# Kernel tuning notes

Measured on AMD Instinct MI355X. Metric: run time of the kernel, lower is better.

## Reference

```python
import jax, jax.numpy as jnp
import numpy as np

N = 50000   # drug nodes
R = 8       # relations (= n_classes)
E = 200000  # edges per relation
ED = 400000 # decoder edges


def _deg_norm(idx, n):
    deg = jax.ops.segment_sum(jnp.ones(idx.shape, jnp.float32), idx, num_segments=n)
    return jnp.where(deg > 0, jax.lax.rsqrt(jnp.maximum(deg, 1.0)), 0.0)


def hetero_conv(x, src, dst, W, b, n):
    # DGL HeteroGraphConv(sum) of GraphConv(norm='both') per relation, single node type.
    out = jnp.zeros((n, W.shape[2]), x.dtype)
    for r in range(W.shape[0]):
        s, d = src[r], dst[r]
        ns = _deg_norm(s, n)  # out-degree^{-1/2} (src norm)
        nd = _deg_norm(d, n)  # in-degree^{-1/2} (dst norm)
        m = (x * ns[:, None]) @ W[r]                       # [n, dout]
        agg = jax.ops.segment_sum(m[s], d, num_segments=n)  # gather+scatter [E, dout]
        out = out + agg * nd[:, None] + b[r]
    return out


def hgcn_layer(x, src, dst, Wa, ba, Wb, bb, n):
    h = hetero_conv(x, src, dst, Wa, ba, n)
    h = jax.nn.relu(h)
    return hetero_conv(h, src, dst, Wb, bb, n)


def setup_inputs() -> dict:
    key = jax.random.key(0)
    ks = jax.random.split(key, 16)
    s = 0.02
    return {
        "node2_features": jax.random.normal(ks[0], (N, 256), jnp.float32),
        "mpnn_features": jax.random.normal(ks[1], (N, 300), jnp.float32),
        "src": jax.random.randint(ks[2], (R, E), 0, N, jnp.int32),
        "dst": jax.random.randint(ks[3], (R, E), 0, N, jnp.int32),
        "dec_src": jax.random.randint(ks[4], (ED,), 0, N, jnp.int32),
        "dec_dst": jax.random.randint(ks[5], (ED,), 0, N, jnp.int32),
        "W2a": jax.random.normal(ks[6], (R, 256, 256), jnp.float32) * s,
        "b2a": jnp.zeros((R, 256), jnp.float32),
        "W2b": jax.random.normal(ks[7], (R, 256, 128), jnp.float32) * s,
        "b2b": jnp.zeros((R, 128), jnp.float32),
        "W3a": jax.random.normal(ks[8], (R, 300, 256), jnp.float32) * s,
        "b3a": jnp.zeros((R, 256), jnp.float32),
        "W3b": jax.random.normal(ks[9], (R, 256, 128), jnp.float32) * s,
        "b3b": jnp.zeros((R, 128), jnp.float32),
        "Wp1": jax.random.normal(ks[10], (512, 256), jnp.float32) * s,
        "bp1": jnp.zeros((256,), jnp.float32),
        "Wp2": jax.random.normal(ks[11], (256, R), jnp.float32) * s,
        "bp2": jnp.zeros((R,), jnp.float32),
    }


def reference(node2_features, mpnn_features, src, dst, dec_src, dec_dst,
              W2a, b2a, W2b, b2b, W3a, b3a, W3b, b3b, Wp1, bp1, Wp2, bp2):
    h2 = hgcn_layer(node2_features, src, dst, W2a, b2a, W2b, b2b, N)  # [N, 128]
    h3 = hgcn_layer(mpnn_features, src, dst, W3a, b3a, W3b, b3b, N)   # [N, 128]
    feat = jnp.concatenate([h2, h3], axis=1)                            # [N, 256]
    # edge-wise gather-concat-MLP (note: original has NO relu between W1 and W2)
    x = jnp.concatenate([feat[dec_src], feat[dec_dst]], axis=1)          # [ED, 512]
    score = (x @ Wp1 + bp1) @ Wp2 + bp2                                  # [ED, R]
    return score
```

## Files before the change

### kernel.cpp

```cpp
#include <hip/hip_runtime.h>
#include <hip/hip_bf16.h>

#define NN 50000
#define RR 8
#define EE 200000
#define EDD 400000
#define SCB 196
#define CH 5000
#define CHK 16

typedef __attribute__((ext_vector_type(8))) short short8;
typedef __attribute__((ext_vector_type(4))) float floatx4;

static __device__ __forceinline__ unsigned short f2bf(float f) {
    union { float f; unsigned u; } v; v.f = f;
    unsigned r = v.u + 0x7fff + ((v.u >> 16) & 1);
    return (unsigned short)(r >> 16);
}
static __device__ __forceinline__ float bf2f(unsigned short h) {
    union { unsigned u; float f; } v; v.u = ((unsigned)h) << 16;
    return v.f;
}
static __device__ __forceinline__ void gload_lds16(const unsigned short* g, unsigned short* l) {
    __builtin_amdgcn_global_load_lds(
        (const __attribute__((address_space(1))) void*)g,
        (__attribute__((address_space(3))) void*)l,
        16, 0, 0);
}

__global__ __launch_bounds__(256) void k_histp(const int* __restrict__ src, const int* __restrict__ dst,
                                               unsigned char* __restrict__ tmp) {
    __shared__ unsigned lh[12512];
    int chunk = blockIdx.x, r = blockIdx.y, which = blockIdx.z;
    const int* idx = (which ? dst : src) + (size_t)r * EE;
    for (int i = threadIdx.x; i < 12512; i += 256) lh[i] = 0;
    __syncthreads();
    int e0 = chunk * (EE / CHK);
    for (int e = e0 + threadIdx.x; e < e0 + EE / CHK; e += 256) {
        int n = idx[e];
        atomicAdd(&lh[n >> 2], 1u << ((n & 3) * 8));
    }
    __syncthreads();
    unsigned* t = (unsigned*)(tmp + (((size_t)(which * RR + r) * CHK + chunk) * 50048));
    for (int i = threadIdx.x; i < 12512; i += 256) t[i] = lh[i];
}

__global__ void k_reduce(const unsigned char* __restrict__ tmp,
                         int* __restrict__ outdeg, int* __restrict__ indeg) {
    int i = blockIdx.x * 256 + threadIdx.x;
    if (i >= 2 * RR * 12512) return;
    int wr = i / 12512;
    int wd = i - wr * 12512;
    unsigned s0 = 0, s1 = 0, s2 = 0, s3 = 0;
    const unsigned* base = (const unsigned*)(tmp + (size_t)wr * CHK * 50048) + wd;
    #pragma unroll
    for (int c = 0; c < CHK; c++) {
        unsigned v = base[(size_t)c * 12512];
        s0 += v & 255u; s1 += (v >> 8) & 255u; s2 += (v >> 16) & 255u; s3 += (v >> 24) & 255u;
    }
    int which = wr / RR, r = wr - which * RR;
    int n = wd * 4;
    int* deg = (which ? indeg : outdeg) + (size_t)r * NN;
    if (n < NN) {
        deg[n] = (int)s0;
        if (n + 1 < NN) deg[n + 1] = (int)s1;
        if (n + 2 < NN) deg[n + 2] = (int)s2;
        if (n + 3 < NN) deg[n + 3] = (int)s3;
    }
}

__global__ void k_norms(int* __restrict__ outdeg, int* __restrict__ indeg) {
    int i = blockIdx.x * blockDim.x + threadIdx.x;
    if (i >= RR * NN) return;
    int od = outdeg[i];
    int id = indeg[i];
    ((float*)outdeg)[i] = od > 0 ? rsqrtf((float)od) : 0.f;
    ((float*)indeg)[i]  = id > 0 ? rsqrtf((float)id) : 0.f;
}

__global__ void k_scanA(const int* __restrict__ indeg, int* __restrict__ bsum) {
    int r = blockIdx.y;
    int i = blockIdx.x * 256 + threadIdx.x;
    int v = (i < NN) ? indeg[(size_t)r * NN + i] : 0;
    #pragma unroll
    for (int d = 32; d > 0; d >>= 1) v += __shfl_down(v, d, 64);
    __shared__ int ws4[4];
    if ((threadIdx.x & 63) == 0) ws4[threadIdx.x >> 6] = v;
    __syncthreads();
    if (threadIdx.x == 0) bsum[r * SCB + blockIdx.x] = ws4[0] + ws4[1] + ws4[2] + ws4[3];
}

__global__ void k_scanB(int* __restrict__ bsum, int* __restrict__ offs) {
    int r = blockIdx.x;
    int t = threadIdx.x;
    int v = (t < SCB) ? bsum[r * SCB + t] : 0;
    int lane = t & 63, wid = t >> 6;
    int sv = v;
    #pragma unroll
    for (int d = 1; d < 64; d <<= 1) {
        int u = __shfl_up(sv, d, 64);
        if (lane >= d) sv += u;
    }
    __shared__ int wsum[4];
    if (lane == 63) wsum[wid] = sv;
    __syncthreads();
    int add = 0;
    for (int x = 0; x < wid; x++) add += wsum[x];
    int incl = sv + add;
    if (t < SCB) bsum[r * SCB + t] = incl - v;
    if (t == 255) offs[(size_t)r * (NN + 1) + NN] = incl;
}

__global__ void k_scanC(const int* __restrict__ indeg, const int* __restrict__ bsum,
                        int* __restrict__ offs) {
    int r = blockIdx.y;
    int i = blockIdx.x * 256 + threadIdx.x;
    int v = (i < NN) ? indeg[(size_t)r * NN + i] : 0;
    int lane = threadIdx.x & 63, wid = threadIdx.x >> 6;
    int sv = v;
    #pragma unroll
    for (int d = 1; d < 64; d <<= 1) {
        int u = __shfl_up(sv, d, 64);
        if (lane >= d) sv += u;
    }
    __shared__ int wsum[4];
    if (lane == 63) wsum[wid] = sv;
    __syncthreads();
    int add = bsum[r * SCB + blockIdx.x];
    for (int x = 0; x < wid; x++) add += wsum[x];
    if (i < NN) offs[(size_t)r * (NN + 1) + i] = sv - v + add;
}

__global__ void k_fillw(const int* __restrict__ src, const int* __restrict__ dst,
                        const int* __restrict__ offs, const float* __restrict__ ns,
                        int* __restrict__ cursor, int2* __restrict__ csrw) {
    int i = blockIdx.x * blockDim.x + threadIdx.x;
    if (i >= RR * EE) return;
    int r = i / EE;
    int s = src[i], d = dst[i];
    int pos = offs[r * (NN + 1) + d] + atomicAdd(&cursor[r * NN + d], 1);
    int2 v;
    v.x = s;
    v.y = __float_as_int(ns[(size_t)r * NN + s]);
    csrw[(size_t)r * EE + pos] = v;
}

__global__ void k_prep(const float* __restrict__ Wp1, const float* __restrict__ Wp2,
                       const float* __restrict__ bp1, const float* __restrict__ bp2,
                       const float* __restrict__ b2a, const float* __restrict__ b2b,
                       const float* __restrict__ b3a, const float* __restrict__ b3b,
                       float* __restrict__ Mcat, float* __restrict__ cvec,
                       float* __restrict__ bs) {
    int bx = blockIdx.x;
    if (bx < 16) {
        int t = bx * 256 + threadIdx.x;
        int i = t >> 4, j = t & 15;
        int half = j >> 3, jj = j & 7;
        const float* wrow = Wp1 + (size_t)(half * 256 + i) * 256;
        float s = 0.f;
        for (int k = 0; k < 256; k++) s += wrow[k] * Wp2[k * 8 + jj];
        Mcat[i * 16 + j] = s;
    } else if (bx == 16) {
        int j = threadIdx.x;
        if (j < 8) {
            float s = bp2[j];
            for (int k = 0; k < 256; k++) s += bp1[k] * Wp2[k * 8 + j];
            cvec[j] = s;
        }
    } else {
        int j = threadIdx.x;
        float s = 0.f;
        for (int r = 0; r < RR; r++) s += b2a[r * 256 + j];
        bs[j] = s;
        if (j < 128) {
            s = 0.f;
            for (int r = 0; r < RR; r++) s += b2b[r * 128 + j];
            bs[256 + j] = s;
        }
        s = 0.f;
        for (int r = 0; r < RR; r++) s += b3a[r * 256 + j];
        bs[512 + j] = s;
        if (j < 128) {
            s = 0.f;
            for (int r = 0; r < RR; r++) s += b3b[r * 128 + j];
            bs[768 + j] = s;
        }
    }
}

__global__ void k_fold(const float* __restrict__ W2b, const float* __restrict__ W3b,
                       const float* __restrict__ Mcat, const float* __restrict__ bs,
                       unsigned short* __restrict__ FmatT, float* __restrict__ cfold) {
    int bx = blockIdx.x;
    if (bx < 256) {
        int idx = bx * 256 + threadIdx.x;
        int rj = idx >> 9, i = idx & 511;
        int r = rj >> 4, j = rj & 15;
        float s = 0.f;
        if (i < 256) {
            const float* wr = W2b + ((size_t)r * 256 + i) * 128;
            for (int c = 0; c < 128; c++) s += wr[c] * Mcat[c * 16 + j];
        } else {
            const float* wr = W3b + ((size_t)r * 256 + (i - 256)) * 128;
            for (int c = 0; c < 128; c++) s += wr[c] * Mcat[(128 + c) * 16 + j];
        }
        FmatT[(size_t)rj * 512 + i] = f2bf(s);
    } else {
        int j = threadIdx.x;
        if (j < 16) {
            float s = 0.f;
            for (int c = 0; c < 128; c++)
                s += bs[256 + c] * Mcat[c * 16 + j] + bs[768 + c] * Mcat[(128 + c) * 16 + j];
            cfold[j] = s;
        }
    }
}

__global__ void k_castx(const float* __restrict__ x2, const float* __restrict__ x3,
                        unsigned short* __restrict__ XH) {
    int i = blockIdx.x * 256 + threadIdx.x;
    if (i >= NN * 560) return;
    int row = i / 560, col = i - row * 560;
    float v;
    if (col < 256) v = x2[(size_t)row * 256 + col];
    else if (col < 556) v = x3[(size_t)row * 300 + (col - 256)];
    else v = 0.f;
    XH[i] = f2bf(v);
}

__global__ void k_wt2(const float* __restrict__ W2a, const float* __restrict__ W3a,
                      unsigned short* __restrict__ WT2, unsigned short* __restrict__ WT3) {
    const float* W; unsigned short* WT; int K0, Kpad;
    if (blockIdx.y == 0) { W = W2a; WT = WT2; K0 = 256; Kpad = 256; }
    else                 { W = W3a; WT = WT3; K0 = 300; Kpad = 304; }
    int i = blockIdx.x * 256 + threadIdx.x;
    int total = 256 * RR * Kpad;
    if (i >= total) return;
    int n = i / (RR * Kpad);
    int rem = i - n * (RR * Kpad);
    int r = rem / Kpad;
    int k = rem - r * Kpad;
    float v = (k < K0) ? W[((size_t)r * K0 + k) * 256 + n] : 0.f;
    WT[i] = f2bf(v);
}

__global__ __launch_bounds__(256) void k_aggp(
        const unsigned short* __restrict__ xb,
        const int2* __restrict__ csrw, const int* __restrict__ offs,
        const float* __restrict__ nd, int nbase,
        unsigned short* __restrict__ Y2, unsigned short* __restrict__ Y3) {
    int lane = threadIdx.x & 63;
    int sub = threadIdx.x >> 6;
    int bn = blockIdx.x * 4 + sub;
    int n = nbase + bn;
    int r = blockIdx.y;
    int o0 = offs[r * (NN + 1) + n];
    int o1 = offs[r * (NN + 1) + n + 1];
    o0 = __builtin_amdgcn_readfirstlane(o0);
    o1 = __builtin_amdgcn_readfirstlane(o1);
    int cnt = o1 - o0;
    float ndv = nd[(size_t)r * NN + n];
    const int2* cs = csrw + (size_t)r * EE + o0;
    bool tl = lane < 6;
    float va[8], vc[8];
    #pragma unroll
    for (int q = 0; q < 8; q++) { va[q] = 0.f; vc[q] = 0.f; }

    for (int eb = 0; eb < cnt; eb += 64) {
        int rem = cnt - eb;
        int2 rec = cs[eb + min(lane, rem - 1)];
        int kmax = rem < 64 ? rem : 64;
        for (int kb = 0; kb < kmax; kb += 4) {
            #pragma unroll
            for (int u = 0; u < 4; u++) {
                int k = kb + u;
                if (k >= kmax) break;
                int sidx = __shfl(rec.x, k, 64);
                float f = __int_as_float(__shfl(rec.y, k, 64));
                const unsigned short* p = xb + (size_t)(unsigned)sidx * 560;
                short8 M = *(const short8*)(p + lane * 8);
                #pragma unroll
                for (int q = 0; q < 8; q++) va[q] += f * bf2f((unsigned short)M[q]);
                if (tl) {
                    short8 C = *(const short8*)(p + 512 + lane * 8);
                    #pragma unroll
                    for (int q = 0; q < 8; q++) vc[q] += f * bf2f((unsigned short)C[q]);
                }
            }
        }
    }
    short8 o;
    #pragma unroll
    for (int q = 0; q < 8; q++) o[q] = (short)f2bf(va[q] * ndv);
    if (lane < 32) {
        *(short8*)(Y2 + (size_t)bn * 2048 + r * 256 + lane * 8) = o;
    } else {
        *(short8*)(Y3 + (size_t)bn * 2432 + r * 304 + (lane - 32) * 8) = o;
    }
    if (tl) {
        short8 oc;
        #pragma unroll
        for (int q = 0; q < 8; q++) oc[q] = (short)f2bf(vc[q] * ndv);
        *(short8*)(Y3 + (size_t)bn * 2432 + r * 304 + 256 + lane * 8) = oc;
    }
}

template<int TN>
__global__ __launch_bounds__(256) void k_gemm_bf(
        const unsigned short* __restrict__ A, int lda,
        const unsigned short* __restrict__ BT, int ldb,
        const float* __restrict__ bias,
        const float* __restrict__ Cin, int ldcin,
        void* __restrict__ Cout, int ldc,
        int M, int K, int flags) {
    constexpr int BN = TN * 32;
    __shared__ unsigned short As[128 * 64];
    __shared__ unsigned short Bs[BN * 64];
    int m0 = blockIdx.x * 128;
    int n0 = blockIdx.y * BN;
    int t = threadIdx.x;
    int w = t >> 6, l = t & 63;
    int qm = (w >> 1) * 64, qn = (w & 1) * (TN * 16);
    int lr = l & 15, lg = l >> 4;
    int lrow = l >> 3;
    int lch  = (l & 7) ^ lrow;

    floatx4 acc[4][TN];
    #pragma unroll
    for (int a = 0; a < 4; a++)
        #pragma unroll
        for (int b = 0; b < TN; b++)
            acc[a][b] = (floatx4){0.f, 0.f, 0.f, 0.f};

    for (int k0 = 0; k0 < K; k0 += 64) {
        #pragma unroll
        for (int j = 0; j < 4; j++) {
            int seg = w * 4 + j;
            int gr = m0 + seg * 8 + lrow; if (gr > M - 1) gr = M - 1;
            gload_lds16(A + (size_t)gr * lda + k0 + lch * 8, &As[seg * 512]);
        }
        #pragma unroll
        for (int j = 0; j < TN; j++) {
            int seg = w * TN + j;
            int row = n0 + seg * 8 + lrow;
            gload_lds16(BT + (size_t)row * ldb + k0 + lch * 8, &Bs[seg * 512]);
        }
        __syncthreads();
        #pragma unroll
        for (int ks = 0; ks < 2; ks++) {
            int slot = ((ks * 4 + lg) ^ (lr & 7)) * 8;
            short8 af[4], bf[TN];
            #pragma unroll
            for (int i = 0; i < 4; i++)
                af[i] = *(const short8*)&As[(qm + i * 16 + lr) * 64 + slot];
            #pragma unroll
            for (int i = 0; i < TN; i++)
                bf[i] = *(const short8*)&Bs[(qn + i * 16 + lr) * 64 + slot];
            #pragma unroll
            for (int tm = 0; tm < 4; tm++)
                #pragma unroll
                for (int tn = 0; tn < TN; tn++)
                    acc[tm][tn] = __builtin_amdgcn_mfma_f32_16x16x32_bf16(
                        af[tm], bf[tn], acc[tm][tn], 0, 0, 0);
        }
        __syncthreads();
    }

    int addbias = flags & 1, accum = flags & 2, relu = flags & 4, outbf = flags & 8;
    #pragma unroll
    for (int tm = 0; tm < 4; tm++) {
        int rbase = m0 + qm + tm * 16 + lg * 4;
        #pragma unroll
        for (int reg = 0; reg < 4; reg++) {
            int row = rbase + reg;
            if (row >= M) continue;
            #pragma unroll
            for (int tn = 0; tn < TN; tn++) {
                int col = n0 + qn + tn * 16 + lr;
                float v = acc[tm][tn][reg];
                if (addbias) v += bias[col];
                if (accum) v += Cin[(size_t)row * ldcin + col];
                if (relu) v = fmaxf(v, 0.f);
                if (outbf) ((unsigned short*)Cout)[(size_t)row * ldc + col] = f2bf(v);
                else       ((float*)Cout)[(size_t)row * ldc + col] = v;
            }
        }
    }
}

__global__ __launch_bounds__(256) void k_gemm2(
        const unsigned short* __restrict__ Y2, const unsigned short* __restrict__ Y3,
        const unsigned short* __restrict__ WT2, const unsigned short* __restrict__ WT3,
        const float* __restrict__ bs, unsigned short* __restrict__ hb,
        int nbase, int M) {
    __shared__ unsigned short As[64 * 64];
    __shared__ unsigned short Bs[64 * 64];
    int x = blockIdx.x;
    int g = (x >> 5) * 8 + (x & 7);
    int nb = (x >> 3) & 3;
    if (g >= 158) return;
    int z = g / 79;
    int mb = g - z * 79;
    const unsigned short* A  = z ? Y3 : Y2;
    const unsigned short* BT = z ? WT3 : WT2;
    int lda = z ? 2432 : 2048;
    int K = lda;
    const float* bias = bs + z * 512;
    int m0 = mb * 64;
    int n0 = nb * 64;
    int t = threadIdx.x;
    int w = t >> 6, l = t & 63;
    int qm = (w >> 1) * 32, qn = (w & 1) * 32;
    int lr = l & 15, lg = l >> 4;
    int lrow = l >> 3;
    int lch  = (l & 7) ^ lrow;

    floatx4 acc[2][2];
    #pragma unroll
    for (int a = 0; a < 2; a++)
        #pragma unroll
        for (int b = 0; b < 2; b++)
            acc[a][b] = (floatx4){0.f, 0.f, 0.f, 0.f};

    for (int k0 = 0; k0 < K; k0 += 64) {
        #pragma unroll
        for (int j = 0; j < 2; j++) {
            int seg = w * 2 + j;
            int gr = m0 + seg * 8 + lrow; if (gr > M - 1) gr = M - 1;
            gload_lds16(A + (size_t)gr * lda + k0 + lch * 8, &As[seg * 512]);
        }
        #pragma unroll
        for (int j = 0; j < 2; j++) {
            int seg = w * 2 + j;
            int row = n0 + seg * 8 + lrow;
            gload_lds16(BT + (size_t)row * lda + k0 + lch * 8, &Bs[seg * 512]);
        }
        __syncthreads();
        #pragma unroll
        for (int ks = 0; ks < 2; ks++) {
            int slot = ((ks * 4 + lg) ^ (lr & 7)) * 8;
            short8 af[2], bf[2];
            #pragma unroll
            for (int i = 0; i < 2; i++)
                af[i] = *(const short8*)&As[(qm + i * 16 + lr) * 64 + slot];
            #pragma unroll
            for (int i = 0; i < 2; i++)
                bf[i] = *(const short8*)&Bs[(qn + i * 16 + lr) * 64 + slot];
            #pragma unroll
            for (int tm = 0; tm < 2; tm++)
                #pragma unroll
                for (int tn = 0; tn < 2; tn++)
                    acc[tm][tn] = __builtin_amdgcn_mfma_f32_16x16x32_bf16(
                        af[tm], bf[tn], acc[tm][tn], 0, 0, 0);
        }
        __syncthreads();
    }

    #pragma unroll
    for (int tm = 0; tm < 2; tm++) {
        int rbase = m0 + qm + tm * 16 + lg * 4;
        #pragma unroll
        for (int reg = 0; reg < 4; reg++) {
            int row = rbase + reg;
            if (row >= M) continue;
            #pragma unroll
            for (int tn = 0; tn < 2; tn++) {
                int col = n0 + qn + tn * 16 + lr;
                float v = fmaxf(acc[tm][tn][reg] + bias[col], 0.f);
                hb[(size_t)(nbase + row) * 512 + z * 256 + col] = f2bf(v);
            }
        }
    }
}

__global__ __launch_bounds__(256) void k_aggAB(
        const int2* __restrict__ csrw, const int* __restrict__ offs,
        const float* __restrict__ nd, const float* __restrict__ G,
        const float* __restrict__ cfold, const float* __restrict__ cvec,
        float* __restrict__ AB) {
    int lane = threadIdx.x & 63, sub = threadIdx.x >> 6;
    int n = blockIdx.x * 4 + sub;
    int slot = lane >> 4, j = lane & 15;
    int jb = slot << 4;
    float acc = 0.f;
    for (int hh = 0; hh < 2; hh++) {
        int r = slot + hh * 4;
        int o0 = offs[r * (NN + 1) + n];
        int o1 = offs[r * (NN + 1) + n + 1];
        float ndv = nd[(size_t)r * NN + n];
        const int2* cs = csrw + (size_t)r * EE + o0;
        int cnt = o1 - o0;
        float t0 = 0.f, t1 = 0.f;
        for (int eb = 0; eb < cnt; eb += 16) {
            int rem = cnt - eb;
            int2 rec = cs[eb + min(j, rem - 1)];
            int kmax = rem < 16 ? rem : 16;
            for (int k = 0; k < kmax; k += 2) {
                int s0 = __shfl(rec.x, jb + k, 64);
                float f0 = __int_as_float(__shfl(rec.y, jb + k, 64));
                int k1 = k + 1 < kmax ? k + 1 : kmax - 1;
                int s1 = __shfl(rec.x, jb + k1, 64);
                float f1 = (k + 1 < kmax) ? __int_as_float(__shfl(rec.y, jb + k1, 64)) : 0.f;
                t0 += f0 * G[(size_t)(unsigned)s0 * 128 + r * 16 + j];
                t1 += f1 * G[(size_t)(unsigned)s1 * 128 + r * 16 + j];
            }
        }
        acc += ndv * (t0 + t1);
    }
    acc += __shfl_xor(acc, 16, 64);
    acc += __shfl_xor(acc, 32, 64);
    if (lane < 16) AB[(size_t)n * 16 + j] = acc + cfold[j] + (j < 8 ? cvec[j] : 0.f);
}

__global__ void k_dec(const int* __restrict__ dsrc, const int* __restrict__ ddst,
                      const float* __restrict__ AB, float* __restrict__ out) {
    int e = blockIdx.x * 256 + threadIdx.x;
    if (e >= EDD) return;
    int s = dsrc[e], d = ddst[e];
    const float4* as = (const float4*)(AB + (size_t)s * 16);
    const float4* ad = (const float4*)(AB + (size_t)d * 16 + 8);
    float4 x0 = as[0], x1 = as[1], y0 = ad[0], y1 = ad[1];
    float4 o0 = {x0.x + y0.x, x0.y + y0.y, x0.z + y0.z, x0.w + y0.w};
    float4 o1 = {x1.x + y1.x, x1.y + y1.y, x1.z + y1.z, x1.w + y1.w};
    float4* op = (float4*)(out + (size_t)e * 8);
    op[0] = o0; op[1] = o1;
}

extern "C" void kernel_launch(void* const* d_in, const int* in_sizes, int n_in,
                              void* d_out, int out_size, void* d_ws, size_t ws_size,
                              hipStream_t stream) {
    const float* x2  = (const float*)d_in[0];
    const float* x3  = (const float*)d_in[1];
    const int*   src = (const int*)d_in[2];
    const int*   dst = (const int*)d_in[3];
    const int*   dsrc = (const int*)d_in[4];
    const int*   ddst = (const int*)d_in[5];
    const float* W2a = (const float*)d_in[6];
    const float* b2a = (const float*)d_in[7];
    const float* W2b = (const float*)d_in[8];
    const float* b2b = (const float*)d_in[9];
    const float* W3a = (const float*)d_in[10];
    const float* b3a = (const float*)d_in[11];
    const float* W3b = (const float*)d_in[12];
    const float* b3b = (const float*)d_in[13];
    const float* Wp1 = (const float*)d_in[14];
    const float* bp1 = (const float*)d_in[15];
    const float* Wp2 = (const float*)d_in[16];
    const float* bp2 = (const float*)d_in[17];
    float* out = (float*)d_out;

    char* ws = (char*)d_ws;
    size_t off = 0;
    auto alloc = [&](size_t nbytes) {
        char* p = ws + off;
        off += nbytes;
        off = (off + 255) & ~(size_t)255;
        return p;
    };
    float* ns   = (float*)alloc((size_t)RR * NN * 4);
    float* nd   = (float*)alloc((size_t)RR * NN * 4);
    int*   offs = (int*)alloc((size_t)RR * (NN + 1) * 4);
    int2*  csrw = (int2*)alloc((size_t)RR * EE * 8);
    unsigned short* XH     = (unsigned short*)alloc((size_t)NN * 560 * 2);
    unsigned short* hbuf23 = (unsigned short*)alloc((size_t)NN * 512 * 2);
    unsigned short* WT2a   = (unsigned short*)alloc((size_t)256 * 2048 * 2);
    unsigned short* WT3a   = (unsigned short*)alloc((size_t)256 * 2432 * 2);
    unsigned short* FmatT  = (unsigned short*)alloc((size_t)128 * 512 * 2);
    char* YR = alloc((size_t)CH * (2048 + 2432) * 2);
    float* Mcat  = (float*)alloc(4096 * 4);
    float* cvec  = (float*)alloc(64 * 4);
    float* bsums = (float*)alloc(1024 * 4);
    float* cfold = (float*)alloc(64 * 4);
    int*   bsum  = (int*)alloc((size_t)RR * SCB * 4);

    unsigned short* Y2a = (unsigned short*)YR;
    unsigned short* Y3a = Y2a + (size_t)CH * 2048;
    int*   outdeg = (int*)ns;
    int*   indeg  = (int*)nd;
    int*   cursor = (int*)YR;
    unsigned char* htmp = (unsigned char*)(YR + (4 << 20));
    float* G      = (float*)YR;
    float* AB     = (float*)(YR + (size_t)NN * 128 * 4);

    hipMemsetAsync(cursor, 0, (size_t)RR * NN * 4, stream);

    k_histp<<<dim3(CHK, RR, 2), 256, 0, stream>>>(src, dst, htmp);
    k_reduce<<<(2 * RR * 12512 + 255) / 256, 256, 0, stream>>>(htmp, outdeg, indeg);
    k_scanA<<<dim3(SCB, RR), 256, 0, stream>>>(indeg, bsum);
    k_scanB<<<RR, 256, 0, stream>>>(bsum, offs);
    k_scanC<<<dim3(SCB, RR), 256, 0, stream>>>(indeg, bsum, offs);
    k_norms<<<(RR * NN + 255) / 256, 256, 0, stream>>>(outdeg, indeg);
    int edgeBlocks = (RR * EE + 255) / 256;
    k_fillw<<<edgeBlocks, 256, 0, stream>>>(src, dst, offs, ns, cursor, csrw);
    k_prep<<<18, 256, 0, stream>>>(Wp1, Wp2, bp1, bp2, b2a, b2b, b3a, b3b, Mcat, cvec, bsums);
    k_fold<<<257, 256, 0, stream>>>(W2b, W3b, Mcat, bsums, FmatT, cfold);

    k_castx<<<(NN * 560 + 255) / 256, 256, 0, stream>>>(x2, x3, XH);
    k_wt2<<<dim3((256 * RR * 304 + 255) / 256, 2), 256, 0, stream>>>(W2a, W3a, WT2a, WT3a);

    for (int c = 0; c < NN / CH; c++) {
        k_aggp<<<dim3(CH / 4, RR), 256, 0, stream>>>(XH, csrw, offs, nd, c * CH, Y2a, Y3a);
        k_gemm2<<<640, 256, 0, stream>>>(
            Y2a, Y3a, WT2a, WT3a, bsums, hbuf23, c * CH, CH);
    }

    k_gemm_bf<1><<<dim3((NN + 127) / 128, 4), 256, 0, stream>>>(
        hbuf23, 512, FmatT, 512, bsums, (const float*)nullptr, 0,
        (void*)G, 128, NN, 512, 0);

    k_aggAB<<<NN / 4, 256, 0, stream>>>(csrw, offs, nd, G, cfold, cvec, AB);
    k_dec<<<(EDD + 255) / 256, 256, 0, stream>>>(dsrc, ddst, AB, out);
}
```

Measured before the change: 1.054 ms.

## Partition CSR fill by dst range, vectorize input cast, batch aggregation loads

The CSR fill kernel now gives each block a range of destination nodes and a chunk of edges, reading src/dst as int4. This localizes the atomics and scattered writes but has each block scan many edges it filters out. The input cast to bf16 now handles eight elements per thread with float4 loads and a single 16-byte store. The aggregation inner loop issues four independent gathered row loads before accumulating, to raise memory-level parallelism, at the cost of more registers and redundant loads for tail edges.

```diff
diff --git a/kernel.cpp b/kernel.cpp
--- a/kernel.cpp
+++ b/kernel.cpp
@@ -131,18 +131,34 @@
     if (i < NN) offs[(size_t)r * (NN + 1) + i] = sv - v + add;
 }
 
-__global__ void k_fillw(const int* __restrict__ src, const int* __restrict__ dst,
-                        const int* __restrict__ offs, const float* __restrict__ ns,
-                        int* __restrict__ cursor, int2* __restrict__ csrw) {
-    int i = blockIdx.x * blockDim.x + threadIdx.x;
-    if (i >= RR * EE) return;
-    int r = i / EE;
-    int s = src[i], d = dst[i];
-    int pos = offs[r * (NN + 1) + d] + atomicAdd(&cursor[r * NN + d], 1);
-    int2 v;
-    v.x = s;
-    v.y = __float_as_int(ns[(size_t)r * NN + s]);
-    csrw[(size_t)r * EE + pos] = v;
+__global__ __launch_bounds__(256) void k_fillw3(const int* __restrict__ src, const int* __restrict__ dst,
+                                                const int* __restrict__ offs, const float* __restrict__ ns,
+                                                int* __restrict__ cursor, int2* __restrict__ csrw) {
+    int range = blockIdx.x, r = blockIdx.y, chunk = blockIdx.z;
+    int lo = range * 6250;
+    const int4* sp = (const int4*)(src + (size_t)r * EE);
+    const int4* dp = (const int4*)(dst + (size_t)r * EE);
+    const int* offr = offs + r * (NN + 1);
+    const float* nsr = ns + (size_t)r * NN;
+    int* cur = cursor + r * NN;
+    int2* cw = csrw + (size_t)r * EE;
+    int e40 = chunk * (EE / 32);
+    for (int e4 = e40 + threadIdx.x; e4 < e40 + EE / 32; e4 += 256) {
+        int4 d4 = dp[e4];
+        int4 s4 = sp[e4];
+        #pragma unroll
+        for (int u = 0; u < 4; u++) {
+            int d = (u == 0 ? d4.x : u == 1 ? d4.y : u == 2 ? d4.z : d4.w) - lo;
+            if ((unsigned)d < 6250u) {
+                int s = (u == 0 ? s4.x : u == 1 ? s4.y : u == 2 ? s4.z : s4.w);
+                int pos = offr[lo + d] + atomicAdd(&cur[lo + d], 1);
+                int2 v;
+                v.x = s;
+                v.y = __float_as_int(nsr[s]);
+                cw[pos] = v;
+            }
+        }
+    }
 }
 
 __global__ void k_prep(const float* __restrict__ Wp1, const float* __restrict__ Wp2,
@@ -219,13 +235,30 @@
 __global__ void k_castx(const float* __restrict__ x2, const float* __restrict__ x3,
                         unsigned short* __restrict__ XH) {
     int i = blockIdx.x * 256 + threadIdx.x;
-    if (i >= NN * 560) return;
-    int row = i / 560, col = i - row * 560;
-    float v;
-    if (col < 256) v = x2[(size_t)row * 256 + col];
-    else if (col < 556) v = x3[(size_t)row * 300 + (col - 256)];
-    else v = 0.f;
-    XH[i] = f2bf(v);
+    if (i >= NN * 70) return;
+    int row = i / 70, oc = (i - row * 70) * 8;
+    short8 o;
+    if (oc < 256) {
+        const float4* p = (const float4*)(x2 + (size_t)row * 256 + oc);
+        float4 a = p[0], b = p[1];
+        o[0] = (short)f2bf(a.x); o[1] = (short)f2bf(a.y);
+        o[2] = (short)f2bf(a.z); o[3] = (short)f2bf(a.w);
+        o[4] = (short)f2bf(b.x); o[5] = (short)f2bf(b.y);
+        o[6] = (short)f2bf(b.z); o[7] = (short)f2bf(b.w);
+    } else if (oc < 552) {
+        const float4* p = (const float4*)(x3 + (size_t)row * 300 + (oc - 256));
+        float4 a = p[0], b = p[1];
+        o[0] = (short)f2bf(a.x); o[1] = (short)f2bf(a.y);
+        o[2] = (short)f2bf(a.z); o[3] = (short)f2bf(a.w);
+        o[4] = (short)f2bf(b.x); o[5] = (short)f2bf(b.y);
+        o[6] = (short)f2bf(b.z); o[7] = (short)f2bf(b.w);
+    } else {
+        const float* p = x3 + (size_t)row * 300 + 296;
+        o[0] = (short)f2bf(p[0]); o[1] = (short)f2bf(p[1]);
+        o[2] = (short)f2bf(p[2]); o[3] = (short)f2bf(p[3]);
+        o[4] = 0; o[5] = 0; o[6] = 0; o[7] = 0;
+    }
+    *(short8*)(XH + (size_t)row * 560 + oc) = o;
 }
 
 __global__ void k_wt2(const float* __restrict__ W2a, const float* __restrict__ W3a,
@@ -271,20 +304,46 @@
         int2 rec = cs[eb + min(lane, rem - 1)];
         int kmax = rem < 64 ? rem : 64;
         for (int kb = 0; kb < kmax; kb += 4) {
-            #pragma unroll
-            for (int u = 0; u < 4; u++) {
-                int k = kb + u;
-                if (k >= kmax) break;
-                int sidx = __shfl(rec.x, k, 64);
-                float f = __int_as_float(__shfl(rec.y, k, 64));
-                const unsigned short* p = xb + (size_t)(unsigned)sidx * 560;
-                short8 M = *(const short8*)(p + lane * 8);
+            int l1 = kb + 1 < kmax ? kb + 1 : kmax - 1;
+            int l2 = kb + 2 < kmax ? kb + 2 : kmax - 1;
+            int l3 = kb + 3 < kmax ? kb + 3 : kmax - 1;
+            int s0 = __shfl(rec.x, kb, 64);
+            int s1 = __shfl(rec.x, l1, 64);
+            int s2 = __shfl(rec.x, l2, 64);
+            int s3 = __shfl(rec.x, l3, 64);
+            float f0 = __int_as_float(__shfl(rec.y, kb, 64));
+            float f1 = kb + 1 < kmax ? __int_as_float(__shfl(rec.y, l1, 64)) : 0.f;
+            float f2 = kb + 2 < kmax ? __int_as_float(__shfl(rec.y, l2, 64)) : 0.f;
+            float f3 = kb + 3 < kmax ? __int_as_float(__shfl(rec.y, l3, 64)) : 0.f;
+            const unsigned short* p0 = xb + (size_t)(unsigned)s0 * 560 + lane * 8;
+            const unsigned short* p1 = xb + (size_t)(unsigned)s1 * 560 + lane * 8;
+            const unsigned short* p2 = xb + (size_t)(unsigned)s2 * 560 + lane * 8;
+            const unsigned short* p3 = xb + (size_t)(unsigned)s3 * 560 + lane * 8;
+            short8 A0 = *(const short8*)p0;
+            short8 A1 = *(const short8*)p1;
+            short8 A2 = *(const short8*)p2;
+            short8 A3 = *(const short8*)p3;
+            short8 C0 = {}, C1 = {}, C2 = {}, C3 = {};
+            if (tl) {
+                C0 = *(const short8*)(p0 + 512);
+                C1 = *(const short8*)(p1 + 512);
+                C2 = *(const short8*)(p2 + 512);
+                C3 = *(const short8*)(p3 + 512);
+            }
+            #pragma unroll
+            for (int q = 0; q < 8; q++) {
+                va[q] += f0 * bf2f((unsigned short)A0[q]);
+                va[q] += f1 * bf2f((unsigned short)A1[q]);
+                va[q] += f2 * bf2f((unsigned short)A2[q]);
+                va[q] += f3 * bf2f((unsigned short)A3[q]);
+            }
+            if (tl) {
                 #pragma unroll
-                for (int q = 0; q < 8; q++) va[q] += f * bf2f((unsigned short)M[q]);
-                if (tl) {
-                    short8 C = *(const short8*)(p + 512 + lane * 8);
-                    #pragma unroll
-                    for (int q = 0; q < 8; q++) vc[q] += f * bf2f((unsigned short)C[q]);
+                for (int q = 0; q < 8; q++) {
+                    vc[q] += f0 * bf2f((unsigned short)C0[q]);
+                    vc[q] += f1 * bf2f((unsigned short)C1[q]);
+                    vc[q] += f2 * bf2f((unsigned short)C2[q]);
+                    vc[q] += f3 * bf2f((unsigned short)C3[q]);
                 }
             }
         }
@@ -590,12 +649,11 @@
     k_scanB<<<RR, 256, 0, stream>>>(bsum, offs);
     k_scanC<<<dim3(SCB, RR), 256, 0, stream>>>(indeg, bsum, offs);
     k_norms<<<(RR * NN + 255) / 256, 256, 0, stream>>>(outdeg, indeg);
-    int edgeBlocks = (RR * EE + 255) / 256;
-    k_fillw<<<edgeBlocks, 256, 0, stream>>>(src, dst, offs, ns, cursor, csrw);
+    k_fillw3<<<dim3(8, RR, 8), 256, 0, stream>>>(src, dst, offs, ns, cursor, csrw);
     k_prep<<<18, 256, 0, stream>>>(Wp1, Wp2, bp1, bp2, b2a, b2b, b3a, b3b, Mcat, cvec, bsums);
     k_fold<<<257, 256, 0, stream>>>(W2b, W3b, Mcat, bsums, FmatT, cfold);
 
-    k_castx<<<(NN * 560 + 255) / 256, 256, 0, stream>>>(x2, x3, XH);
+    k_castx<<<(NN * 70 + 255) / 256, 256, 0, stream>>>(x2, x3, XH);
     k_wt2<<<dim3((256 * RR * 304 + 255) / 256, 2), 256, 0, stream>>>(W2a, W3a, WT2a, WT3a);
 
     for (int c = 0; c < NN / CH; c++) {
```

Result: no change. 1.052 ms (-0.2%).
